# Kernel tuning notes

Measured on AMD Instinct MI355X. Metric: run time of the kernel, lower is better.

The kernel has to match this reference:

```python
import jax, jax.numpy as jnp
import numpy as np

NUM_HEADS = 16
D_MODEL = 1024


def setup_inputs() -> dict:
    key = jax.random.key(0)
    ks = jax.random.split(key, 12)
    B, S, D = 2, 2048, D_MODEL
    inp = {
        "query": jax.random.normal(ks[0], (B, S, D), dtype=jnp.float32),
        "key": jax.random.normal(ks[1], (B, S, D), dtype=jnp.float32),
        "value": jax.random.normal(ks[2], (B, S, D), dtype=jnp.float32),
        "mask": jax.random.randint(ks[3], (B, 1, S), 0, 2).astype(jnp.bool_),
    }
    # Linear layer params, stored as (in, out) so y = x @ W + b
    sd = 1.0 / np.sqrt(D)
    for i, nm in enumerate(["q", "k", "v", "o"]):
        inp[f"W{nm}"] = jax.random.uniform(ks[4 + 2 * i], (D, D), jnp.float32, -sd, sd)
        inp[f"b{nm}"] = jax.random.uniform(ks[5 + 2 * i], (D,), jnp.float32, -sd, sd)
    return inp


def _split_heads(x):
    # [B, S, D] -> [B, H, S, d_k]
    B, S, D = x.shape
    return x.reshape(B, S, NUM_HEADS, D // NUM_HEADS).transpose(0, 2, 1, 3)


def reference(query, key, value, mask, Wq, bq, Wk, bk, Wv, bv, Wo, bo):
    B, Sq, D = query.shape
    d_k = D // NUM_HEADS
    scale = 1.0 / np.sqrt(d_k)

    q = _split_heads(query @ Wq + bq)   # [B,H,Sq,dk]
    k = _split_heads(key @ Wk + bk)     # [B,H,Sk,dk]
    v = _split_heads(value @ Wv + bv)   # [B,H,Sk,dk]

    scores = jnp.einsum("bhqd,bhkd->bhqk", q, k) * scale  # [B,H,Sq,Sk]
    # mask: [B,1,Sk] bool, True = masked; broadcast over heads and queries
    scores = jnp.where(mask[:, None, :, :], -jnp.inf, scores)
    attn = jax.nn.softmax(scores, axis=-1)
    attn = jnp.nan_to_num(attn, nan=0.0)  # fully-masked rows -> 0 (matches torch)

    ctx = jnp.einsum("bhqk,bhkd->bhqd", attn, v)  # [B,H,Sq,dk]
    ctx = ctx.transpose(0, 2, 1, 3).reshape(B, Sq, D)  # combine heads
    out = ctx @ Wo + bo
    return out
```

## Files before the change

### kernel.cpp

```cpp
#include <hip/hip_runtime.h>


typedef unsigned short u16;
typedef __attribute__((ext_vector_type(8))) short bf16x8;
typedef __attribute__((ext_vector_type(4))) float f32x4;

static __device__ __forceinline__ u16 f2bf(float x) {
  union { float f; unsigned int i; } v; v.f = x;
  return (u16)((v.i + 0x8000u) >> 16);
}

#define MFMA_B16(a, b, c) __builtin_amdgcn_mfma_f32_16x16x32_bf16((a), (b), (c), 0, 0, 0)

__global__ __launch_bounds__(256) void prep_w(
    const float* __restrict__ w0, const float* __restrict__ w1,
    const float* __restrict__ w2, const float* __restrict__ w3,
    u16* __restrict__ t0, u16* __restrict__ t1,
    u16* __restrict__ t2, u16* __restrict__ t3) {
  __shared__ u16 tile[64 * 68];
  const float* W; u16* T;
  switch (blockIdx.z) {
    case 0: W = w0; T = t0; break;
    case 1: W = w1; T = t1; break;
    case 2: W = w2; T = t2; break;
    default: W = w3; T = t3; break;
  }
  const int t = threadIdx.x;
  const int k0 = blockIdx.x * 64, n0 = blockIdx.y * 64;
#pragma unroll
  for (int it = 0; it < 4; ++it) {
    int idx = it * 256 + t;
    int r = idx >> 4, c4 = idx & 15;
    float4 v = *(const float4*)&W[(size_t)(k0 + r) * 1024 + n0 + c4 * 4];
    tile[r * 68 + c4 * 4 + 0] = f2bf(v.x);
    tile[r * 68 + c4 * 4 + 1] = f2bf(v.y);
    tile[r * 68 + c4 * 4 + 2] = f2bf(v.z);
    tile[r * 68 + c4 * 4 + 3] = f2bf(v.w);
  }
  __syncthreads();
#pragma unroll
  for (int it = 0; it < 2; ++it) {
    int idx = it * 256 + t;
    int n = idx >> 3, kc = idx & 7;
    bf16x8 pk;
#pragma unroll
    for (int j = 0; j < 8; ++j) pk[j] = (short)tile[(kc * 8 + j) * 68 + n];
    *(bf16x8*)&T[(size_t)(n0 + n) * 1024 + k0 + kc * 8] = pk;
  }
}

template <int MT, int AMODE, int OMODE>
__global__ __launch_bounds__(256) void gemm_bias(
    const void* a0v, const void* a1v, const void* a2v,
    const u16* __restrict__ Wt,
    const float* b0, const float* b1, const float* b2,
    void* o0, void* o1, void* o2) {
  __shared__ __align__(16) u16 As[MT * 32 * 32];
  __shared__ __align__(16) u16 Bs[128 * 32];
  const int t = threadIdx.x, wave = t >> 6, lane = t & 63;
  const int l15 = lane & 15, quad = lane >> 4;
  const int m0 = blockIdx.x * (MT * 32);
  const int n0 = blockIdx.y * 128;
  const int rg = (OMODE == 3) ? (n0 >> 10) : 0;
  const void* Av = (rg == 0) ? a0v : (rg == 1 ? a1v : a2v);
  const float* bp = (rg == 0) ? b0 : (rg == 1 ? b1 : b2);
  const int nb = (OMODE == 3) ? (n0 & 1023) : n0;
  const int wr = (wave >> 1) * (MT * 16), wc = (wave & 1) * 64;

  const f32x4 fz = {0.f, 0.f, 0.f, 0.f};
  f32x4 acc[MT][4];
#pragma unroll
  for (int mt = 0; mt < MT; ++mt)
#pragma unroll
    for (int nt = 0; nt < 4; ++nt) acc[mt][nt] = fz;

  float4 pa[MT / 2][2]; bf16x8 pab[MT / 2]; bf16x8 pb[2];
#pragma unroll
  for (int s = 0; s < MT / 2; ++s) {
    int idx = s * 256 + t, row = idx >> 2, seg = idx & 3;
    if (AMODE == 1) {
      const float* ap = (const float*)Av + (size_t)(m0 + row) * 1024 + seg * 8;
      pa[s][0] = *(const float4*)ap; pa[s][1] = *(const float4*)(ap + 4);
    } else {
      pab[s] = *(const bf16x8*)((const u16*)Av + (size_t)(m0 + row) * 1024 + seg * 8);
    }
  }
#pragma unroll
  for (int s = 0; s < 2; ++s) {
    int idx = s * 256 + t, row = idx >> 2, seg = idx & 3;
    pb[s] = *(const bf16x8*)&Wt[(size_t)(n0 + row) * 1024 + seg * 8];
  }

  for (int kb = 0; kb < 1024; kb += 32) {
    __syncthreads();
#pragma unroll
    for (int s = 0; s < MT / 2; ++s) {
      int idx = s * 256 + t, row = idx >> 2, seg = idx & 3;
      bf16x8 pk;
      if (AMODE == 1) {
        pk[0] = (short)f2bf(pa[s][0].x); pk[1] = (short)f2bf(pa[s][0].y);
        pk[2] = (short)f2bf(pa[s][0].z); pk[3] = (short)f2bf(pa[s][0].w);
        pk[4] = (short)f2bf(pa[s][1].x); pk[5] = (short)f2bf(pa[s][1].y);
        pk[6] = (short)f2bf(pa[s][1].z); pk[7] = (short)f2bf(pa[s][1].w);
      } else pk = pab[s];
      *(bf16x8*)&As[row * 32 + seg * 8] = pk;
    }
#pragma unroll
    for (int s = 0; s < 2; ++s) {
      int idx = s * 256 + t, row = idx >> 2, seg = idx & 3;
      *(bf16x8*)&Bs[row * 32 + seg * 8] = pb[s];
    }
    __syncthreads();
    const int kn = (kb + 32) & 1023;
#pragma unroll
    for (int s = 0; s < MT / 2; ++s) {
      int idx = s * 256 + t, row = idx >> 2, seg = idx & 3;
      if (AMODE == 1) {
        const float* ap = (const float*)Av + (size_t)(m0 + row) * 1024 + kn + seg * 8;
        pa[s][0] = *(const float4*)ap; pa[s][1] = *(const float4*)(ap + 4);
      } else {
        pab[s] = *(const bf16x8*)((const u16*)Av + (size_t)(m0 + row) * 1024 + kn + seg * 8);
      }
    }
#pragma unroll
    for (int s = 0; s < 2; ++s) {
      int idx = s * 256 + t, row = idx >> 2, seg = idx & 3;
      pb[s] = *(const bf16x8*)&Wt[(size_t)(n0 + row) * 1024 + kn + seg * 8];
    }
    bf16x8 a[MT], bfr[4];
#pragma unroll
    for (int mt = 0; mt < MT; ++mt)
      a[mt] = *(const bf16x8*)&As[(wr + mt * 16 + l15) * 32 + quad * 8];
#pragma unroll
    for (int nt = 0; nt < 4; ++nt)
      bfr[nt] = *(const bf16x8*)&Bs[(wc + nt * 16 + l15) * 32 + quad * 8];
#pragma unroll
    for (int mt = 0; mt < MT; ++mt)
#pragma unroll
      for (int nt = 0; nt < 4; ++nt)
        acc[mt][nt] = MFMA_B16(a[mt], bfr[nt], acc[mt][nt]);
  }

#pragma unroll
  for (int nt = 0; nt < 4; ++nt) {
    const int n = nb + wc + nt * 16 + l15;
    const float bv = bp[n];
#pragma unroll
    for (int mt = 0; mt < MT; ++mt)
#pragma unroll
      for (int r = 0; r < 4; ++r) {
        const int m = m0 + wr + mt * 16 + quad * 4 + r;
        const float val = acc[mt][nt][r] + bv;
        if (OMODE == 2) {
          ((float*)o0)[(size_t)m * 1024 + n] = val;
        } else if (OMODE == 0) {
          ((u16*)o0)[(size_t)m * 1024 + n] = f2bf(val);
        } else {
          if (rg == 0)      ((u16*)o0)[(size_t)m * 1024 + n] = f2bf(val);
          else if (rg == 1) ((u16*)o1)[(size_t)m * 1024 + n] = f2bf(val);
          else {
            const int h = n >> 6, d = n & 63, bb = m >> 11, ss = m & 2047;
            ((u16*)o2)[((size_t)(bb * 16 + h) * 64 + d) * 2048 + ss] = f2bf(val);
          }
        }
      }
  }
}

__global__ __launch_bounds__(256) void attn_fused(
    const u16* Q, const u16* __restrict__ K,
    const u16* __restrict__ Vt, const int* __restrict__ mask,
    u16* ctx) {
  __shared__ __align__(16) u16 Ks[64 * 72];
  __shared__ __align__(16) u16 Vs[64 * 72];
  __shared__ __align__(16) u16 Pl[4][16 * 72];
  __shared__ u16 Ms[2048];
  const int t = threadIdx.x, wave = t >> 6, lane = t & 63;
  const int l15 = lane & 15, quad = lane >> 4;
  const int bh = blockIdx.y, b = bh >> 4, h = bh & 15;
  const int q0 = blockIdx.x * 64 + wave * 16;
  const float cs = 0.125f * 1.44269504f;

#pragma unroll
  for (int i = 0; i < 8; ++i)
    Ms[i * 256 + t] = (u16)(mask[b * 2048 + i * 256 + t] ? 1 : 0);

  const u16* Qp = Q + (size_t)(b * 2048 + q0) * 1024 + h * 64;
  const bf16x8 qf0 = *(const bf16x8*)(Qp + (size_t)l15 * 1024 + quad * 8);
  const bf16x8 qf1 = *(const bf16x8*)(Qp + (size_t)l15 * 1024 + 32 + quad * 8);

  const u16* Kbase = K + (size_t)(b * 2048) * 1024 + h * 64;
  const u16* Vbase = Vt + (size_t)bh * 64 * 2048;

  const int r0 = t >> 3, c0 = (t & 7) * 8;
  const int r1 = 32 + r0;

  bf16x8 gk0 = *(const bf16x8*)&Kbase[(size_t)r0 * 1024 + c0];
  bf16x8 gk1 = *(const bf16x8*)&Kbase[(size_t)r1 * 1024 + c0];
  bf16x8 gv0 = *(const bf16x8*)&Vbase[(size_t)r0 * 2048 + c0];
  bf16x8 gv1 = *(const bf16x8*)&Vbase[(size_t)r1 * 2048 + c0];

  const f32x4 fz = {0.f, 0.f, 0.f, 0.f};
  f32x4 o[4];
  f32x4 lpart = fz;
#pragma unroll
  for (int i = 0; i < 4; ++i) o[i] = fz;

  for (int kt = 0; kt < 2048; kt += 64) {
    __syncthreads();
    *(bf16x8*)&Ks[r0 * 72 + c0] = gk0;
    *(bf16x8*)&Ks[r1 * 72 + c0] = gk1;
    *(bf16x8*)&Vs[r0 * 72 + c0] = gv0;
    *(bf16x8*)&Vs[r1 * 72 + c0] = gv1;
    __syncthreads();
    const int kn = (kt + 64) & 2047;
    gk0 = *(const bf16x8*)&Kbase[(size_t)(kn + r0) * 1024 + c0];
    gk1 = *(const bf16x8*)&Kbase[(size_t)(kn + r1) * 1024 + c0];
    gv0 = *(const bf16x8*)&Vbase[(size_t)r0 * 2048 + kn + c0];
    gv1 = *(const bf16x8*)&Vbase[(size_t)r1 * 2048 + kn + c0];

    f32x4 s[4];
#pragma unroll
    for (int nt = 0; nt < 4; ++nt) {
      const int krow = nt * 16 + l15;
      bf16x8 k0 = *(const bf16x8*)&Ks[krow * 72 + quad * 8];
      bf16x8 k1 = *(const bf16x8*)&Ks[krow * 72 + 32 + quad * 8];
      f32x4 acc = MFMA_B16(qf0, k0, fz);
      acc = MFMA_B16(qf1, k1, acc);
      const int mv = (int)Ms[kt + krow];
#pragma unroll
      for (int r = 0; r < 4; ++r) {
        float p = mv ? 0.f : exp2f(fminf(acc[r] * cs, 80.f));
        s[nt][r] = p; lpart[r] += p;
      }
    }
#pragma unroll
    for (int nt = 0; nt < 4; ++nt)
#pragma unroll
      for (int r = 0; r < 4; ++r)
        Pl[wave][(quad * 4 + r) * 72 + nt * 16 + l15] = f2bf(s[nt][r]);
#pragma unroll
    for (int kc = 0; kc < 2; ++kc) {
      const bf16x8 pf = *(const bf16x8*)&Pl[wave][l15 * 72 + kc * 32 + quad * 8];
#pragma unroll
      for (int nt = 0; nt < 4; ++nt) {
        const bf16x8 vf = *(const bf16x8*)&Vs[(nt * 16 + l15) * 72 + kc * 32 + quad * 8];
        o[nt] = MFMA_B16(pf, vf, o[nt]);
      }
    }
  }
  float lrow[4];
#pragma unroll
  for (int r = 0; r < 4; ++r) {
    float sl = lpart[r];
    sl += __shfl_xor(sl, 1);
    sl += __shfl_xor(sl, 2);
    sl += __shfl_xor(sl, 4);
    sl += __shfl_xor(sl, 8);
    lrow[r] = sl;
  }
  u16* cp = ctx + (size_t)(b * 2048 + q0) * 1024 + h * 64;
#pragma unroll
  for (int r = 0; r < 4; ++r) {
    const bool ok = lrow[r] > 0.f;
    const float inv = ok ? 1.f / lrow[r] : 0.f;
#pragma unroll
    for (int nt = 0; nt < 4; ++nt)
      cp[(quad * 4 + r) * 1024 + nt * 16 + l15] = f2bf(ok ? o[nt][r] * inv : 0.f);
  }
}

extern "C" void kernel_launch(void* const* d_in, const int* in_sizes, int n_in,
                              void* d_out, int out_size, void* d_ws, size_t ws_size,
                              hipStream_t stream) {
  const float* q    = (const float*)d_in[0];
  const float* k    = (const float*)d_in[1];
  const float* v    = (const float*)d_in[2];
  const int*   mask = (const int*)d_in[3];
  const float* Wq = (const float*)d_in[4];  const float* bq = (const float*)d_in[5];
  const float* Wk = (const float*)d_in[6];  const float* bk = (const float*)d_in[7];
  const float* Wv = (const float*)d_in[8];  const float* bv = (const float*)d_in[9];
  const float* Wo = (const float*)d_in[10]; const float* bo = (const float*)d_in[11];

  char* ws = (char*)d_ws;
  u16*   Kp  = (u16*)(ws + ((size_t)0 << 20));
  u16*   Vt  = (u16*)(ws + ((size_t)8 << 20));
  float* O32 = (float*)ws;

  char* od = (char*)d_out;
  u16* ctx = (u16*)od;
  u16* WqT = (u16*)(od + ((size_t)8 << 20));
  u16* WkT = (u16*)(od + ((size_t)10 << 20));
  u16* WvT = (u16*)(od + ((size_t)12 << 20));
  u16* WoT = (u16*)(od + ((size_t)14 << 20));

  dim3 blk(256);
  prep_w<<<dim3(16, 16, 4), blk, 0, stream>>>(Wq, Wk, Wv, Wo, WqT, WkT, WvT, WoT);
  gemm_bias<4, 1, 3><<<dim3(32, 24), blk, 0, stream>>>(
      q, k, v, WqT, bq, bk, bv, (void*)ctx, (void*)Kp, (void*)Vt);
  attn_fused<<<dim3(32, 32), blk, 0, stream>>>(ctx, Kp, Vt, mask, ctx);
  gemm_bias<2, 0, 2><<<dim3(64, 8), blk, 0, stream>>>(
      ctx, nullptr, nullptr, WoT, bo, nullptr, nullptr, (void*)O32, nullptr, nullptr);
  hipMemcpyAsync(d_out, O32, (size_t)out_size * sizeof(float),
                 hipMemcpyDeviceToDevice, stream);
}
```

Before: 277.0 us.

## Enlarge attention tiles to 128 queries and 128 keys with 8-wave blocks

The attention kernel now runs 512-thread blocks covering 128 queries and stages 128 keys of K and V per iteration, which halves the number of barrier-separated loop trips and doubles reuse of each K/V tile across waves. The mask is stored as a bf16 bias (-inf or 0) and folded into an fma before exp2, replacing the branch and the clamp. This costs more shared memory and registers per block and launches half as many blocks, which may lower occupancy. Removing the clamp also drops the guard against overflow in exp2.

```diff
diff --git a/kernel.cpp b/kernel.cpp
--- a/kernel.cpp
+++ b/kernel.cpp
@@ -8,6 +8,9 @@
 static __device__ __forceinline__ u16 f2bf(float x) {
   union { float f; unsigned int i; } v; v.f = x;
   return (u16)((v.i + 0x8000u) >> 16);
+}
+static __device__ __forceinline__ float bf2f(u16 u) {
+  union { unsigned int i; float f; } v; v.i = ((unsigned int)u) << 16; return v.f;
 }
 
 #define MFMA_B16(a, b, c) __builtin_amdgcn_mfma_f32_16x16x32_bf16((a), (b), (c), 0, 0, 0)
@@ -167,23 +170,25 @@
   }
 }
 
-__global__ __launch_bounds__(256) void attn_fused(
+__global__ __launch_bounds__(512) void attn_fused(
     const u16* Q, const u16* __restrict__ K,
     const u16* __restrict__ Vt, const int* __restrict__ mask,
     u16* ctx) {
-  __shared__ __align__(16) u16 Ks[64 * 72];
-  __shared__ __align__(16) u16 Vs[64 * 72];
-  __shared__ __align__(16) u16 Pl[4][16 * 72];
-  __shared__ u16 Ms[2048];
+  __shared__ __align__(16) u16 Ks[128 * 72];
+  __shared__ __align__(16) u16 Vs[64 * 136];
+  __shared__ __align__(16) u16 Pl[8][16 * 136];
+  __shared__ u16 Mb[2048];
   const int t = threadIdx.x, wave = t >> 6, lane = t & 63;
   const int l15 = lane & 15, quad = lane >> 4;
   const int bh = blockIdx.y, b = bh >> 4, h = bh & 15;
-  const int q0 = blockIdx.x * 64 + wave * 16;
+  const int q0 = blockIdx.x * 128 + wave * 16;
   const float cs = 0.125f * 1.44269504f;
 
 #pragma unroll
-  for (int i = 0; i < 8; ++i)
-    Ms[i * 256 + t] = (u16)(mask[b * 2048 + i * 256 + t] ? 1 : 0);
+  for (int i = 0; i < 4; ++i) {
+    int idx = i * 512 + t;
+    Mb[idx] = mask[b * 2048 + idx] ? 0xFF80 : 0;
+  }
 
   const u16* Qp = Q + (size_t)(b * 2048 + q0) * 1024 + h * 64;
   const bf16x8 qf0 = *(const bf16x8*)(Qp + (size_t)l15 * 1024 + quad * 8);
@@ -192,13 +197,15 @@
   const u16* Kbase = K + (size_t)(b * 2048) * 1024 + h * 64;
   const u16* Vbase = Vt + (size_t)bh * 64 * 2048;
 
-  const int r0 = t >> 3, c0 = (t & 7) * 8;
-  const int r1 = 32 + r0;
-
-  bf16x8 gk0 = *(const bf16x8*)&Kbase[(size_t)r0 * 1024 + c0];
-  bf16x8 gk1 = *(const bf16x8*)&Kbase[(size_t)r1 * 1024 + c0];
-  bf16x8 gv0 = *(const bf16x8*)&Vbase[(size_t)r0 * 2048 + c0];
-  bf16x8 gv1 = *(const bf16x8*)&Vbase[(size_t)r1 * 2048 + c0];
+  const int kr0 = t >> 3,        kc0 = (t & 7) * 8;
+  const int kr1 = (512 + t) >> 3;
+  const int vr0 = t >> 4,        vc0 = (t & 15) * 8;
+  const int vr1 = (512 + t) >> 4;
+
+  bf16x8 gk0 = *(const bf16x8*)&Kbase[(size_t)kr0 * 1024 + kc0];
+  bf16x8 gk1 = *(const bf16x8*)&Kbase[(size_t)kr1 * 1024 + kc0];
+  bf16x8 gv0 = *(const bf16x8*)&Vbase[(size_t)vr0 * 2048 + vc0];
+  bf16x8 gv1 = *(const bf16x8*)&Vbase[(size_t)vr1 * 2048 + vc0];
 
   const f32x4 fz = {0.f, 0.f, 0.f, 0.f};
   f32x4 o[4];
@@ -206,45 +213,45 @@
 #pragma unroll
   for (int i = 0; i < 4; ++i) o[i] = fz;
 
-  for (int kt = 0; kt < 2048; kt += 64) {
+  for (int kt = 0; kt < 2048; kt += 128) {
     __syncthreads();
-    *(bf16x8*)&Ks[r0 * 72 + c0] = gk0;
-    *(bf16x8*)&Ks[r1 * 72 + c0] = gk1;
-    *(bf16x8*)&Vs[r0 * 72 + c0] = gv0;
-    *(bf16x8*)&Vs[r1 * 72 + c0] = gv1;
+    *(bf16x8*)&Ks[kr0 * 72 + kc0] = gk0;
+    *(bf16x8*)&Ks[kr1 * 72 + kc0] = gk1;
+    *(bf16x8*)&Vs[vr0 * 136 + vc0] = gv0;
+    *(bf16x8*)&Vs[vr1 * 136 + vc0] = gv1;
     __syncthreads();
-    const int kn = (kt + 64) & 2047;
-    gk0 = *(const bf16x8*)&Kbase[(size_t)(kn + r0) * 1024 + c0];
-    gk1 = *(const bf16x8*)&Kbase[(size_t)(kn + r1) * 1024 + c0];
-    gv0 = *(const bf16x8*)&Vbase[(size_t)r0 * 2048 + kn + c0];
-    gv1 = *(const bf16x8*)&Vbase[(size_t)r1 * 2048 + kn + c0];
-
-    f32x4 s[4];
-#pragma unroll
-    for (int nt = 0; nt < 4; ++nt) {
+    const int kn = (kt + 128) & 2047;
+    gk0 = *(const bf16x8*)&Kbase[(size_t)(kn + kr0) * 1024 + kc0];
+    gk1 = *(const bf16x8*)&Kbase[(size_t)(kn + kr1) * 1024 + kc0];
+    gv0 = *(const bf16x8*)&Vbase[(size_t)vr0 * 2048 + kn + vc0];
+    gv1 = *(const bf16x8*)&Vbase[(size_t)vr1 * 2048 + kn + vc0];
+
+    float pv[8][4];
+#pragma unroll
+    for (int nt = 0; nt < 8; ++nt) {
       const int krow = nt * 16 + l15;
       bf16x8 k0 = *(const bf16x8*)&Ks[krow * 72 + quad * 8];
       bf16x8 k1 = *(const bf16x8*)&Ks[krow * 72 + 32 + quad * 8];
       f32x4 acc = MFMA_B16(qf0, k0, fz);
       acc = MFMA_B16(qf1, k1, acc);
-      const int mv = (int)Ms[kt + krow];
+      const float bias = bf2f(Mb[kt + krow]);
 #pragma unroll
       for (int r = 0; r < 4; ++r) {
-        float p = mv ? 0.f : exp2f(fminf(acc[r] * cs, 80.f));
-        s[nt][r] = p; lpart[r] += p;
+        float p = exp2f(fmaf(acc[r], cs, bias));
+        pv[nt][r] = p; lpart[r] += p;
       }
     }
 #pragma unroll
-    for (int nt = 0; nt < 4; ++nt)
+    for (int nt = 0; nt < 8; ++nt)
 #pragma unroll
       for (int r = 0; r < 4; ++r)
-        Pl[wave][(quad * 4 + r) * 72 + nt * 16 + l15] = f2bf(s[nt][r]);
-#pragma unroll
-    for (int kc = 0; kc < 2; ++kc) {
-      const bf16x8 pf = *(const bf16x8*)&Pl[wave][l15 * 72 + kc * 32 + quad * 8];
+        Pl[wave][(quad * 4 + r) * 136 + nt * 16 + l15] = f2bf(pv[nt][r]);
+#pragma unroll
+    for (int kc = 0; kc < 4; ++kc) {
+      const bf16x8 pf = *(const bf16x8*)&Pl[wave][l15 * 136 + kc * 32 + quad * 8];
 #pragma unroll
       for (int nt = 0; nt < 4; ++nt) {
-        const bf16x8 vf = *(const bf16x8*)&Vs[(nt * 16 + l15) * 72 + kc * 32 + quad * 8];
+        const bf16x8 vf = *(const bf16x8*)&Vs[(nt * 16 + l15) * 136 + kc * 32 + quad * 8];
         o[nt] = MFMA_B16(pf, vf, o[nt]);
       }
     }
@@ -298,7 +305,7 @@
   prep_w<<<dim3(16, 16, 4), blk, 0, stream>>>(Wq, Wk, Wv, Wo, WqT, WkT, WvT, WoT);
   gemm_bias<4, 1, 3><<<dim3(32, 24), blk, 0, stream>>>(
       q, k, v, WqT, bq, bk, bv, (void*)ctx, (void*)Kp, (void*)Vt);
-  attn_fused<<<dim3(32, 32), blk, 0, stream>>>(ctx, Kp, Vt, mask, ctx);
+  attn_fused<<<dim3(16, 32), dim3(512), 0, stream>>>(ctx, Kp, Vt, mask, ctx);
   gemm_bias<2, 0, 2><<<dim3(64, 8), blk, 0, stream>>>(
       ctx, nullptr, nullptr, WoT, bo, nullptr, nullptr, (void*)O32, nullptr, nullptr);
   hipMemcpyAsync(d_out, O32, (size_t)out_size * sizeof(float),
```

Result: faster. 267.8 us (-3.3%).
